# Kernel tuning notes

Hardware: AMD Instinct MI355X
Metric: run time of the kernel (lower is better)

## Reference

```python
import jax, jax.numpy as jnp
import numpy as np

FIELD_DIMS = [40000] * 26
OUTPUT_DIM = 1
FEATURE_DIM = int(np.sum(FIELD_DIMS))  # 1_040_000
BATCH = 65536
NUM_FIELDS = len(FIELD_DIMS)


def setup_inputs() -> dict:
    key = jax.random.key(0)
    kx, kw = jax.random.split(key)
    # per-field indices in [0, field_dim)
    x = jax.random.randint(kx, (BATCH, NUM_FIELDS), 0, 40000, dtype=jnp.int64 if jax.config.jax_enable_x64 else jnp.int32)
    # offsets: start of each field in the flattened feature space
    offsets = jnp.asarray(np.concatenate([[0], np.cumsum(FIELD_DIMS)[:-1]]), dtype=x.dtype)
    # nn.Linear weight is (output_dim, feature_dim); store transposed for gather: (feature_dim, output_dim)
    W = 0.01 * jax.random.normal(kw, (FEATURE_DIM, OUTPUT_DIM), dtype=jnp.float32)
    b = jnp.zeros((OUTPUT_DIM,), dtype=jnp.float32)
    return {"x": x, "offsets": offsets, "W": W, "b": b}


def reference(x, offsets, W, b):
    # one-hot scatter + dense Linear == gather rows of W at offset-adjusted ids and sum over fields
    idx = x + offsets[None, :]            # (B, F)
    rows = W[idx]                          # (B, F, output_dim)
    return rows.sum(axis=1) + b            # (B, output_dim)
```

## Files before the change

kernel.cpp:

```cpp
#include <hip/hip_runtime.h>
#include <hip/hip_bf16.h>


#define NUM_FIELDS 26
#define BATCH 65536

__global__ __launch_bounds__(256) void FeaturesLinear_kernel(
    const int* __restrict__ x,
    const int* __restrict__ offsets,
    const float* __restrict__ W,
    const float* __restrict__ bias,
    float* __restrict__ out,
    int batch) {
  int b = blockIdx.x * blockDim.x + threadIdx.x;
  if (b >= batch) return;

  const int* xr = x + b * NUM_FIELDS;

  int idx[NUM_FIELDS];
#pragma unroll
  for (int f = 0; f < NUM_FIELDS; ++f) {
    idx[f] = xr[f] + offsets[f];
  }

  float s = 0.f;
#pragma unroll
  for (int f = 0; f < NUM_FIELDS; ++f) {
    s += W[idx[f]];
  }

  out[b] = s + bias[0];
}

extern "C" void kernel_launch(void* const* d_in, const int* in_sizes, int n_in,
                              void* d_out, int out_size, void* d_ws, size_t ws_size,
                              hipStream_t stream) {
  const int* x = (const int*)d_in[0];
  const int* offsets = (const int*)d_in[1];
  const float* W = (const float*)d_in[2];
  const float* bias = (const float*)d_in[3];
  float* out = (float*)d_out;

  int batch = in_sizes[0] / NUM_FIELDS;

  dim3 block(256);
  dim3 grid((batch + 255) / 256);
  FeaturesLinear_kernel<<<grid, block, 0, stream>>>(x, offsets, W, bias, out, batch);
}
```

Measured before the change: 73.13 us.

## Assign one 32-lane group per batch row with shuffle reduction

Each batch row is now handled by 32 lanes instead of one thread. Each lane loads one field index, so reads of x are coalesced across the group and the 26 gathers are spread over lanes. A shuffle-xor tree then sums the values. This removes the strided per-thread loads of x and the serial dependent gathers, at the cost of 6 idle lanes per group, launching 32x more threads, and adding shuffle overhead.

After: 75.88 us. 3.8% more time.

```diff
diff --git a/kernel.cpp b/kernel.cpp
--- a/kernel.cpp
+++ b/kernel.cpp
@@ -3,7 +3,6 @@
 
 
 #define NUM_FIELDS 26
-#define BATCH 65536
 
 __global__ __launch_bounds__(256) void FeaturesLinear_kernel(
     const int* __restrict__ x,
@@ -12,24 +11,19 @@
     const float* __restrict__ bias,
     float* __restrict__ out,
     int batch) {
-  int b = blockIdx.x * blockDim.x + threadIdx.x;
-  if (b >= batch) return;
+  const int l = threadIdx.x & 31;
+  const int row = (blockIdx.x * blockDim.x + threadIdx.x) >> 5;
+  if (row >= batch) return;
 
-  const int* xr = x + b * NUM_FIELDS;
+  const int lc = (l < NUM_FIELDS) ? l : (NUM_FIELDS - 1);
+  const int idx = x[row * NUM_FIELDS + lc] + offsets[lc];
+  float v = W[idx];
+  if (l >= NUM_FIELDS) v = 0.f;
 
-  int idx[NUM_FIELDS];
 #pragma unroll
-  for (int f = 0; f < NUM_FIELDS; ++f) {
-    idx[f] = xr[f] + offsets[f];
-  }
+  for (int m = 16; m > 0; m >>= 1) v += __shfl_xor(v, m, 32);
 
-  float s = 0.f;
-#pragma unroll
-  for (int f = 0; f < NUM_FIELDS; ++f) {
-    s += W[idx[f]];
-  }
-
-  out[b] = s + bias[0];
+  if (l == 0) out[row] = v + bias[0];
 }
 
 extern "C" void kernel_launch(void* const* d_in, const int* in_sizes, int n_in,
@@ -43,7 +37,8 @@
 
   int batch = in_sizes[0] / NUM_FIELDS;
 
-  dim3 block(256);
-  dim3 grid((batch + 255) / 256);
-  FeaturesLinear_kernel<<<grid, block, 0, stream>>>(x, offsets, W, bias, out, batch);
+  const int block = 256;
+  const int rows_per_block = block / 32;
+  dim3 grid((batch + rows_per_block - 1) / rows_per_block);
+  FeaturesLinear_kernel<<<grid, dim3(block), 0, stream>>>(x, offsets, W, bias, out, batch);
 }
```
